# Kernel optimization log

Hardware: AMD Instinct MI355X
Metric: run time of the kernel (lower is better)

The kernel has to match this reference:

```python
import jax, jax.numpy as jnp
import numpy as np

N = 100000
E = 1600000
ROUND = 2


def spmm(src, dst, x):
    # adj.matmul(x) with binary sparse adjacency given as edge list:
    # out[dst] += x[src]
    return jax.ops.segment_sum(x[src], dst, num_segments=N)


def setup_inputs() -> dict:
    key = jax.random.key(0)
    ks = jax.random.split(key, 8)
    x = jax.random.normal(ks[0], (N, 512), dtype=jnp.float32)
    W_embed = jax.random.normal(ks[1], (512, 64), dtype=jnp.float32) * (1.0 / np.sqrt(512))
    b_embed = jnp.zeros((64,), dtype=jnp.float32)
    W_cls = jax.random.normal(ks[2], (448, 40), dtype=jnp.float32) * (1.0 / np.sqrt(448))
    b_cls = jnp.zeros((40,), dtype=jnp.float32)
    adj_src = jax.random.randint(ks[3], (E,), 0, N, dtype=jnp.int32)
    adj_dst = jax.random.randint(ks[4], (E,), 0, N, dtype=jnp.int32)
    adj2_src = jax.random.randint(ks[5], (E,), 0, N, dtype=jnp.int32)
    adj2_dst = jax.random.randint(ks[6], (E,), 0, N, dtype=jnp.int32)
    return {"x": x, "W_embed": W_embed, "b_embed": b_embed, "W_cls": W_cls,
            "b_cls": b_cls, "adj_src": adj_src, "adj_dst": adj_dst,
            "adj2_src": adj2_src, "adj2_dst": adj2_dst}


def reference(x, W_embed, b_embed, W_cls, b_cls, adj_src, adj_dst, adj2_src, adj2_dst):
    # embed: Linear + ReLU
    h = jax.nn.relu(x @ W_embed + b_embed)  # [N, 64]
    hidden_reps = [h]
    for _ in range(ROUND):
        r1 = spmm(adj_src, adj_dst, h)      # 1-hop aggregation
        r2 = spmm(adj2_src, adj2_dst, h)    # 2-hop aggregation
        h = jnp.concatenate([r1, r2], axis=-1)
        hidden_reps.append(h)
    hf = jnp.concatenate(hidden_reps, axis=-1)  # [N, 64*(2^(ROUND+1)-1)] = [N, 448]
    # dropout is identity in eval mode
    logits = hf @ W_cls + b_cls
    return jax.nn.log_softmax(logits, axis=1)
```

## Files before the change

### kernel.cpp

```cpp
#include <hip/hip_runtime.h>
#include <hip/hip_bf16.h>

#define NN 100000
#define EE 1600000
#define NBK 196
#define BSH 9
#define EPB 4096
#define STG 10240

using frag8 = __attribute__((ext_vector_type(8))) short;
using f32x4 = __attribute__((ext_vector_type(4))) float;

__device__ inline unsigned short f2bf(float f) {
    unsigned u = __float_as_uint(f);
    u = u + 0x7FFFu + ((u >> 16) & 1u);
    return (unsigned short)(u >> 16);
}
__device__ inline float bf2f(unsigned short u) {
    return __uint_as_float(((unsigned)u) << 16);
}
__device__ inline unsigned pack_bf16(float a, float b) {
    __hip_bfloat162 h = __float22bfloat162_rn(float2{a, b});
    union { __hip_bfloat162 h2; unsigned u; } c;
    c.h2 = h;
    return c.u;
}


__global__ __launch_bounds__(256) void bhist_k(const int* __restrict__ d1,
                                               const int* __restrict__ d2,
                                               int* __restrict__ bcnt) {
    __shared__ int lh[NBK];
    int adj = blockIdx.y;
    const int* dd = adj ? d2 : d1;
    int t = threadIdx.x;
    for (int i = t; i < NBK; i += 256) lh[i] = 0;
    __syncthreads();
    int e0 = blockIdx.x * EPB;
    #pragma unroll
    for (int k = 0; k < 16; ++k) {
        int e = e0 + k * 256 + t;
        if (e < EE) atomicAdd(&lh[dd[e] >> BSH], 1);
    }
    __syncthreads();
    for (int i = t; i < NBK; i += 256)
        if (lh[i]) atomicAdd(&bcnt[adj * NBK + i], lh[i]);
}

__global__ __launch_bounds__(256) void bscan_k(const int* __restrict__ bcnt,
                                               int* __restrict__ bbase,
                                               int* __restrict__ bcur) {
    int adj = blockIdx.x;
    __shared__ int s[256];
    int t = threadIdx.x;
    int v = (t < NBK) ? bcnt[adj * NBK + t] : 0;
    s[t] = v;
    __syncthreads();
    for (int off = 1; off < 256; off <<= 1) {
        int u = (t >= off) ? s[t - off] : 0;
        __syncthreads();
        s[t] += u;
        __syncthreads();
    }
    if (t < NBK) {
        int ex = s[t] - v;
        bbase[adj * (NBK + 1) + t] = ex;
        bcur[adj * NBK + t] = ex;
    }
    if (t == NBK - 1) bbase[adj * (NBK + 1) + NBK] = s[t];
}

__global__ __launch_bounds__(256) void binA_k(const int* __restrict__ s1,
                                              const int* __restrict__ d1,
                                              const int* __restrict__ s2,
                                              const int* __restrict__ d2,
                                              int* __restrict__ bcur,
                                              uint2* __restrict__ tmp1,
                                              uint2* __restrict__ tmp2) {
    __shared__ int lhist[NBK], lbase[NBK], gbase[NBK], lcur[NBK];
    __shared__ int sscan[256];
    __shared__ int stot;
    __shared__ uint2 stage[EPB];
    int adj = blockIdx.y;
    const int* ss = adj ? s2 : s1;
    const int* dd = adj ? d2 : d1;
    uint2* tmp = adj ? tmp2 : tmp1;
    int t = threadIdx.x;
    for (int i = t; i < NBK; i += 256) { lhist[i] = 0; lcur[i] = 0; }
    __syncthreads();
    int e0 = blockIdx.x * EPB;
    int d[16], s[16];
    #pragma unroll
    for (int k = 0; k < 16; ++k) {
        int e = e0 + k * 256 + t;
        d[k] = (e < EE) ? dd[e] : -1;
        s[k] = (e < EE) ? ss[e] : 0;
        if (d[k] >= 0) atomicAdd(&lhist[d[k] >> BSH], 1);
    }
    __syncthreads();
    int hv = (t < NBK) ? lhist[t] : 0;
    sscan[t] = hv;
    __syncthreads();
    for (int off = 1; off < 256; off <<= 1) {
        int u = (t >= off) ? sscan[t - off] : 0;
        __syncthreads();
        sscan[t] += u;
        __syncthreads();
    }
    if (t < NBK) lbase[t] = sscan[t] - hv;
    if (t == NBK - 1) stot = sscan[t];
    __syncthreads();
    for (int i = t; i < NBK; i += 256)
        gbase[i] = lhist[i] ? atomicAdd(&bcur[adj * NBK + i], lhist[i]) : 0;
    __syncthreads();
    #pragma unroll
    for (int k = 0; k < 16; ++k) {
        if (d[k] >= 0) {
            int b = d[k] >> BSH;
            int pos = lbase[b] + atomicAdd(&lcur[b], 1);
            stage[pos] = make_uint2((unsigned)d[k], (unsigned)s[k]);
        }
    }
    __syncthreads();
    int tot = stot;
    for (int i = t; i < tot; i += 256) {
        uint2 u = stage[i];
        int b = u.x >> BSH;
        tmp[gbase[b] + (i - lbase[b])] = u;
    }
}

__global__ __launch_bounds__(256) void binB_k(const uint2* __restrict__ tmp1,
                                              const uint2* __restrict__ tmp2,
                                              const int* __restrict__ bbase,
                                              int* __restrict__ rs1,
                                              int* __restrict__ rs2,
                                              int* __restrict__ csr1,
                                              int* __restrict__ csr2) {
    __shared__ int cnt[512], cur[512];
    __shared__ int sscan[256];
    __shared__ int stage[STG];
    int adj = blockIdx.y, b = blockIdx.x;
    const uint2* tmp = adj ? tmp2 : tmp1;
    int* rs  = adj ? rs2  : rs1;
    int* csr = adj ? csr2 : csr1;
    int t = threadIdx.x;
    int n0 = b << BSH;
    int n1 = n0 + 512; if (n1 > NN) n1 = NN;
    int nn = n1 - n0;
    int base = bbase[adj * (NBK + 1) + b];
    int count = bbase[adj * (NBK + 1) + b + 1] - base;
    cnt[t] = 0; cnt[t + 256] = 0;
    __syncthreads();
    for (int i = t; i < count; i += 256)
        atomicAdd(&cnt[tmp[base + i].x - n0], 1);
    __syncthreads();
    int c0 = cnt[2 * t], c1 = cnt[2 * t + 1];
    int ps = c0 + c1;
    sscan[t] = ps;
    __syncthreads();
    for (int off = 1; off < 256; off <<= 1) {
        int u = (t >= off) ? sscan[t - off] : 0;
        __syncthreads();
        sscan[t] += u;
        __syncthreads();
    }
    int pe = sscan[t] - ps;
    int e0x = pe, e1x = pe + c0;
    if (2 * t < nn)     rs[n0 + 2 * t]     = base + e0x;
    if (2 * t + 1 < nn) rs[n0 + 2 * t + 1] = base + e1x;
    cur[2 * t] = e0x; cur[2 * t + 1] = e1x;
    if (t == 0 && n1 == NN) rs[NN] = base + count;
    __syncthreads();
    for (int i = t; i < count; i += 256) {
        uint2 u = tmp[base + i];
        int loc = atomicAdd(&cur[u.x - n0], 1);
        if (loc < STG) stage[loc] = (int)u.y;
        else csr[base + loc] = (int)u.y;
    }
    __syncthreads();
    int m = count < STG ? count : STG;
    for (int i = t; i < m; i += 256) csr[base + i] = stage[i];
}


__global__ void wconv_k(const float* __restrict__ W, unsigned short* __restrict__ Wbf) {
    int id = blockIdx.x * 256 + threadIdx.x;
    if (id < 512 * 64) {
        int k = id >> 6, col = id & 63;
        int ch = k >> 3, el = k & 7;
        int cs = (ch & ~15) | ((ch & 15) ^ (col & 7));
        Wbf[col * 512 + cs * 8 + el] = f2bf(W[id]);
    }
}


__global__ void wcls_k(const float* __restrict__ Wc, unsigned short* __restrict__ Wbig) {
    int id = blockIdx.x * 256 + threadIdx.x;
    int k = id >> 7, col = id & 127;
    float v = 0.f;
    if (col < 40) v = Wc[k * 40 + col];
    else if (col < 80)  { if (k >= 64) v = Wc[(192 + k - 64) * 40 + (col - 40)]; }
    else if (col < 120) { if (k >= 64) v = Wc[(320 + k - 64) * 40 + (col - 80)]; }
    int ch = k >> 3, el = k & 7;
    int phys = (ch & ~7) | ((ch & 7) ^ (col & 7));
    Wbig[col * 192 + phys * 8 + el] = f2bf(v);
}


__global__ __launch_bounds__(256) void embed_k(const float* __restrict__ x,
                                               const unsigned short* __restrict__ Wbf,
                                               const float* __restrict__ bias,
                                               unsigned short* __restrict__ hcat) {
    __shared__ unsigned short sA[64 * 128];
    __shared__ unsigned short sW[64 * 128];
    int tid = threadIdx.x;
    int lane = tid & 63, wave = tid >> 6;
    int row0 = blockIdx.x * 64;
    f32x4 acc[4];
    #pragma unroll
    for (int n = 0; n < 4; n++) acc[n] = (f32x4){0.f, 0.f, 0.f, 0.f};

    int ccol = tid & 15;
    int rbase = tid >> 4;

    for (int kt = 0; kt < 4; ++kt) {
        #pragma unroll
        for (int rr = 0; rr < 4; ++rr) {
            int r = rbase + rr * 16;
            int grow = row0 + r;
            float v[8];
            if (grow < NN) {
                const float4* px = (const float4*)(x + (size_t)grow * 512 + kt * 128 + ccol * 8);
                float4 p0 = px[0], p1 = px[1];
                v[0] = p0.x; v[1] = p0.y; v[2] = p0.z; v[3] = p0.w;
                v[4] = p1.x; v[5] = p1.y; v[6] = p1.z; v[7] = p1.w;
            } else {
                #pragma unroll
                for (int i = 0; i < 8; i++) v[i] = 0.f;
            }
            unsigned uu[4];
            #pragma unroll
            for (int i = 0; i < 4; i++)
                uu[i] = pack_bf16(v[2 * i], v[2 * i + 1]);
            int cs = ccol ^ (r & 7);
            uint4 pk; pk.x = uu[0]; pk.y = uu[1]; pk.z = uu[2]; pk.w = uu[3];
            *(uint4*)&sA[(r * 16 + cs) * 8] = pk;
        }
        for (int q = tid; q < 1024; q += 256) {
            int col = q >> 4, c = q & 15;
            ((uint4*)sW)[q] = ((const uint4*)Wbf)[col * 64 + kt * 16 + c];
        }
        __syncthreads();
        #pragma unroll
        for (int kk = 0; kk < 4; ++kk) {
            int ar = wave * 16 + (lane & 15);
            int ac = (kk * 4 + (lane >> 4)) ^ (ar & 7);
            frag8 a = *(const frag8*)&sA[(ar * 16 + ac) * 8];
            #pragma unroll
            for (int n = 0; n < 4; n++) {
                int col = n * 16 + (lane & 15);
                int bc = (kk * 4 + (lane >> 4)) ^ (col & 7);
                frag8 b = *(const frag8*)&sW[(col * 16 + bc) * 8];
                acc[n] = __builtin_amdgcn_mfma_f32_16x16x32_bf16(a, b, acc[n], 0, 0, 0);
            }
        }
        __syncthreads();
    }
    #pragma unroll
    for (int n = 0; n < 4; n++) {
        int col = n * 16 + (lane & 15);
        float bv = bias[col];
        #pragma unroll
        for (int i = 0; i < 4; i++) {
            int r = row0 + wave * 16 + (lane >> 4) * 4 + i;
            if (r < NN) {
                float vv = acc[n][i] + bv;
                vv = vv > 0.f ? vv : 0.f;
                hcat[(size_t)r * 192 + col] = f2bf(vv);
            }
        }
    }
}


__device__ inline void gacc8(float* a, uint4 u) {
    a[0] += bf2f((unsigned short)(u.x & 0xffff));
    a[1] += bf2f((unsigned short)(u.x >> 16));
    a[2] += bf2f((unsigned short)(u.y & 0xffff));
    a[3] += bf2f((unsigned short)(u.y >> 16));
    a[4] += bf2f((unsigned short)(u.z & 0xffff));
    a[5] += bf2f((unsigned short)(u.z >> 16));
    a[6] += bf2f((unsigned short)(u.w & 0xffff));
    a[7] += bf2f((unsigned short)(u.w >> 16));
}


__global__ __launch_bounds__(256) void round1_k(unsigned short* __restrict__ hc,
                                                const int* __restrict__ rs1,
                                                const int* __restrict__ csr1,
                                                const int* __restrict__ rs2,
                                                const int* __restrict__ csr2) {
    int wave = threadIdx.x >> 6, lane = threadIdx.x & 63;
    int row = blockIdx.x * 4 + wave;
    int g = lane >> 3, gl = lane & 7;

    int s1 = rs1[row], e1 = rs1[row + 1];
    int s2 = rs2[row], e2 = rs2[row + 1];
    int c1 = e1 - s1, c2 = e2 - s2;
    int idx1 = 0, idx2 = 0;
    if (lane < c1) idx1 = csr1[s1 + lane];
    if (lane < c2) idx2 = csr2[s2 + lane];
    int cnt1 = c1 < 64 ? c1 : 64, cnt2 = c2 < 64 ? c2 : 64;

    float a1[8] = {0.f, 0.f, 0.f, 0.f, 0.f, 0.f, 0.f, 0.f};
    float a2[8] = {0.f, 0.f, 0.f, 0.f, 0.f, 0.f, 0.f, 0.f};

    {
        int j0 = g, j1 = 8 + g;
        int x10 = __shfl(idx1, j0), x11 = __shfl(idx1, j1);
        int x20 = __shfl(idx2, j0), x21 = __shfl(idx2, j1);
        uint4 u10 = *(const uint4*)(hc + (size_t)x10 * 192 + gl * 8);
        uint4 u11 = *(const uint4*)(hc + (size_t)x11 * 192 + gl * 8);
        uint4 u20 = *(const uint4*)(hc + (size_t)x20 * 192 + gl * 8);
        uint4 u21 = *(const uint4*)(hc + (size_t)x21 * 192 + gl * 8);
        if (j0 < cnt1) gacc8(a1, u10);
        if (j1 < cnt1) gacc8(a1, u11);
        if (j0 < cnt2) gacc8(a2, u20);
        if (j1 < cnt2) gacc8(a2, u21);
    }
    int nq1 = (cnt1 + 7) >> 3, nq2 = (cnt2 + 7) >> 3;
    int nq = nq1 > nq2 ? nq1 : nq2;
    for (int q = 2; q < nq; ++q) {
        int j = q * 8 + g;
        int y1 = __shfl(idx1, j), y2 = __shfl(idx2, j);
        uint4 v1 = *(const uint4*)(hc + (size_t)y1 * 192 + gl * 8);
        uint4 v2 = *(const uint4*)(hc + (size_t)y2 * 192 + gl * 8);
        if (j < cnt1) gacc8(a1, v1);
        if (j < cnt2) gacc8(a2, v2);
    }
    for (int t0 = s1 + 64; t0 < e1; t0 += 64) {
        int rem = e1 - t0;
        int idxv = 0;
        if (lane < rem) idxv = csr1[t0 + lane];
        int cnt = rem < 64 ? rem : 64;
        int nqt = (cnt + 7) >> 3;
        for (int q = 0; q < nqt; ++q) {
            int j = q * 8 + g;
            int s0 = __shfl(idxv, j);
            uint4 u = *(const uint4*)(hc + (size_t)s0 * 192 + gl * 8);
            if (j < cnt) gacc8(a1, u);
        }
    }
    for (int t0 = s2 + 64; t0 < e2; t0 += 64) {
        int rem = e2 - t0;
        int idxv = 0;
        if (lane < rem) idxv = csr2[t0 + lane];
        int cnt = rem < 64 ? rem : 64;
        int nqt = (cnt + 7) >> 3;
        for (int q = 0; q < nqt; ++q) {
            int j = q * 8 + g;
            int s0 = __shfl(idxv, j);
            uint4 u = *(const uint4*)(hc + (size_t)s0 * 192 + gl * 8);
            if (j < cnt) gacc8(a2, u);
        }
    }

    #pragma unroll
    for (int i = 0; i < 8; ++i) {
        a1[i] += __shfl_xor(a1[i], 8);
        a1[i] += __shfl_xor(a1[i], 16);
        a1[i] += __shfl_xor(a1[i], 32);
        a2[i] += __shfl_xor(a2[i], 8);
        a2[i] += __shfl_xor(a2[i], 16);
        a2[i] += __shfl_xor(a2[i], 32);
    }
    if (lane < 8) {
        uint4 o;
        o.x = pack_bf16(a1[0], a1[1]);
        o.y = pack_bf16(a1[2], a1[3]);
        o.z = pack_bf16(a1[4], a1[5]);
        o.w = pack_bf16(a1[6], a1[7]);
        *(uint4*)(hc + (size_t)row * 192 + 64 + lane * 8) = o;
    } else if (lane < 16) {
        int l = lane - 8;
        uint4 o;
        o.x = pack_bf16(a2[0], a2[1]);
        o.y = pack_bf16(a2[2], a2[3]);
        o.z = pack_bf16(a2[4], a2[5]);
        o.w = pack_bf16(a2[6], a2[7]);
        *(uint4*)(hc + (size_t)row * 192 + 128 + l * 8) = o;
    }
}


__global__ __launch_bounds__(256) void gemm_k(const unsigned short* __restrict__ hcat,
                                              const unsigned short* __restrict__ Wbig,
                                              const float* __restrict__ bc,
                                              float* __restrict__ logits,
                                              unsigned short* __restrict__ zcat) {
    __shared__ unsigned short sA[64 * 64];
    __shared__ unsigned short sB[128 * 64];
    int tid = threadIdx.x;
    int lane = tid & 63, wave = tid >> 6;
    int row0 = blockIdx.x * 64;
    f32x4 acc[8];
    #pragma unroll
    for (int n = 0; n < 8; n++) acc[n] = (f32x4){0.f, 0.f, 0.f, 0.f};

    for (int kt = 0; kt < 3; ++kt) {
        #pragma unroll
        for (int q = tid; q < 512; q += 256) {
            int r = q >> 3, c = q & 7;
            int phys = c ^ (r & 7);
            ((uint4*)sA)[r * 8 + phys] = ((const uint4*)hcat)[(size_t)(row0 + r) * 24 + kt * 8 + c];
        }
        #pragma unroll
        for (int q = tid; q < 1024; q += 256) {
            int col = q >> 3, c = q & 7;
            ((uint4*)sB)[q] = ((const uint4*)Wbig)[col * 24 + kt * 8 + c];
        }
        __syncthreads();
        #pragma unroll
        for (int kk = 0; kk < 2; ++kk) {
            int ar = wave * 16 + (lane & 15);
            int ac = (kk * 4 + (lane >> 4)) ^ (ar & 7);
            frag8 a = *(const frag8*)&sA[(ar * 8 + ac) * 8];
            #pragma unroll
            for (int n = 0; n < 8; n++) {
                int col = n * 16 + (lane & 15);
                int bcc = (kk * 4 + (lane >> 4)) ^ (col & 7);
                frag8 b = *(const frag8*)&sB[(col * 8 + bcc) * 8];
                acc[n] = __builtin_amdgcn_mfma_f32_16x16x32_bf16(a, b, acc[n], 0, 0, 0);
            }
        }
        __syncthreads();
    }
    #pragma unroll
    for (int n = 0; n < 8; n++) {
        int col = n * 16 + (lane & 15);
        float bv = (col < 40) ? bc[col] : 0.f;
        #pragma unroll
        for (int i = 0; i < 4; i++) {
            int r = row0 + wave * 16 + (lane >> 4) * 4 + i;
            if (r < NN) {
                float vv = acc[n][i];
                if (col < 40) {
                    logits[(size_t)r * 40 + col] = vv + bv;
                } else if (col < 80) {
                    zcat[(size_t)r * 128 + (col - 40)] = f2bf(vv);
                } else if (col < 120) {
                    zcat[(size_t)r * 128 + 64 + (col - 80)] = f2bf(vv);
                }
            }
        }
    }
}


__global__ __launch_bounds__(256) void round2_k(const unsigned short* __restrict__ zc,
                                                const int* __restrict__ rs1,
                                                const int* __restrict__ csr1,
                                                const int* __restrict__ rs2,
                                                const int* __restrict__ csr2,
                                                float* __restrict__ logits) {
    int wave = threadIdx.x >> 6, lane = threadIdx.x & 63;
    int row = blockIdx.x * 4 + wave;
    int g = lane >> 3, gl = lane & 7;

    int s1 = rs1[row], e1 = rs1[row + 1];
    int s2 = rs2[row], e2 = rs2[row + 1];
    int c1 = e1 - s1, c2 = e2 - s2;
    int idx1 = 0, idx2 = 0;
    if (lane < c1) idx1 = csr1[s1 + lane];
    if (lane < c2) idx2 = csr2[s2 + lane];
    int cnt1 = c1 < 64 ? c1 : 64, cnt2 = c2 < 64 ? c2 : 64;

    size_t zo1 = gl * 8;
    size_t zo2 = 64 + gl * 8;
    float a[8] = {0.f, 0.f, 0.f, 0.f, 0.f, 0.f, 0.f, 0.f};

    {
        int j0 = g, j1 = 8 + g;
        int x10 = __shfl(idx1, j0), x11 = __shfl(idx1, j1);
        int x20 = __shfl(idx2, j0), x21 = __shfl(idx2, j1);
        uint4 u10 = *(const uint4*)(zc + (size_t)x10 * 128 + zo1);
        uint4 u11 = *(const uint4*)(zc + (size_t)x11 * 128 + zo1);
        uint4 u20 = *(const uint4*)(zc + (size_t)x20 * 128 + zo2);
        uint4 u21 = *(const uint4*)(zc + (size_t)x21 * 128 + zo2);
        if (j0 < cnt1) gacc8(a, u10);
        if (j1 < cnt1) gacc8(a, u11);
        if (j0 < cnt2) gacc8(a, u20);
        if (j1 < cnt2) gacc8(a, u21);
    }
    int nq1 = (cnt1 + 7) >> 3, nq2 = (cnt2 + 7) >> 3;
    int nq = nq1 > nq2 ? nq1 : nq2;
    for (int q = 2; q < nq; ++q) {
        int j = q * 8 + g;
        int y1 = __shfl(idx1, j), y2 = __shfl(idx2, j);
        uint4 v1 = *(const uint4*)(zc + (size_t)y1 * 128 + zo1);
        uint4 v2 = *(const uint4*)(zc + (size_t)y2 * 128 + zo2);
        if (j < cnt1) gacc8(a, v1);
        if (j < cnt2) gacc8(a, v2);
    }
    for (int t0 = s1 + 64; t0 < e1; t0 += 64) {
        int rem = e1 - t0;
        int idxv = 0;
        if (lane < rem) idxv = csr1[t0 + lane];
        int cnt = rem < 64 ? rem : 64;
        int nqt = (cnt + 7) >> 3;
        for (int q = 0; q < nqt; ++q) {
            int j = q * 8 + g;
            int s0 = __shfl(idxv, j);
            uint4 u = *(const uint4*)(zc + (size_t)s0 * 128 + zo1);
            if (j < cnt) gacc8(a, u);
        }
    }
    for (int t0 = s2 + 64; t0 < e2; t0 += 64) {
        int rem = e2 - t0;
        int idxv = 0;
        if (lane < rem) idxv = csr2[t0 + lane];
        int cnt = rem < 64 ? rem : 64;
        int nqt = (cnt + 7) >> 3;
        for (int q = 0; q < nqt; ++q) {
            int j = q * 8 + g;
            int s0 = __shfl(idxv, j);
            uint4 u = *(const uint4*)(zc + (size_t)s0 * 128 + zo2);
            if (j < cnt) gacc8(a, u);
        }
    }

    #pragma unroll
    for (int i = 0; i < 8; ++i) {
        a[i] += __shfl_xor(a[i], 8);
        a[i] += __shfl_xor(a[i], 16);
        a[i] += __shfl_xor(a[i], 32);
    }

    bool act = lane < 5;
    float v[8];
    if (act) {
        float4 b0 = *(const float4*)(logits + (size_t)row * 40 + lane * 8);
        float4 b1 = *(const float4*)(logits + (size_t)row * 40 + lane * 8 + 4);
        v[0] = b0.x + a[0]; v[1] = b0.y + a[1]; v[2] = b0.z + a[2]; v[3] = b0.w + a[3];
        v[4] = b1.x + a[4]; v[5] = b1.y + a[5]; v[6] = b1.z + a[6]; v[7] = b1.w + a[7];
    } else {
        #pragma unroll
        for (int i = 0; i < 8; ++i) v[i] = -1e30f;
    }
    float m = fmaxf(fmaxf(fmaxf(v[0], v[1]), fmaxf(v[2], v[3])),
                    fmaxf(fmaxf(v[4], v[5]), fmaxf(v[6], v[7])));
    m = fmaxf(m, __shfl_xor(m, 1));
    m = fmaxf(m, __shfl_xor(m, 2));
    m = fmaxf(m, __shfl_xor(m, 4));
    float es = 0.f;
    if (act) {
        #pragma unroll
        for (int i = 0; i < 8; ++i) es += __expf(v[i] - m);
    }
    es += __shfl_xor(es, 1);
    es += __shfl_xor(es, 2);
    es += __shfl_xor(es, 4);
    float ls = __logf(es);
    if (act) {
        float4 o0, o1;
        o0.x = v[0] - m - ls; o0.y = v[1] - m - ls; o0.z = v[2] - m - ls; o0.w = v[3] - m - ls;
        o1.x = v[4] - m - ls; o1.y = v[5] - m - ls; o1.z = v[6] - m - ls; o1.w = v[7] - m - ls;
        *(float4*)(logits + (size_t)row * 40 + lane * 8)     = o0;
        *(float4*)(logits + (size_t)row * 40 + lane * 8 + 4) = o1;
    }
}


extern "C" void kernel_launch(void* const* d_in, const int* in_sizes, int n_in,
                              void* d_out, int out_size, void* d_ws, size_t ws_size,
                              hipStream_t stream) {
    const float* x       = (const float*)d_in[0];
    const float* W_embed = (const float*)d_in[1];
    const float* b_embed = (const float*)d_in[2];
    const float* W_cls   = (const float*)d_in[3];
    const float* b_cls   = (const float*)d_in[4];
    const int* a1src = (const int*)d_in[5];
    const int* a1dst = (const int*)d_in[6];
    const int* a2src = (const int*)d_in[7];
    const int* a2dst = (const int*)d_in[8];

    float* logits = (float*)d_out;
    float* ws = (float*)d_ws;

    const size_t OFF_HCAT = 0;
    const size_t OFF_ZCAT = 9600000;
    const size_t OFF_RS1  = 16000000;
    const size_t OFF_RS2  = 16100004;
    const size_t OFF_BB   = 16200008;
    const size_t OFF_BC   = 16200402;
    const size_t OFF_BCNT = 16200794;
    const size_t OFF_CSR1 = 16201188;
    const size_t OFF_CSR2 = 17801188;
    const size_t OFF_WBF  = 19401188;
    const size_t OFF_WBIG = 19417572;

    unsigned short* hcat = (unsigned short*)(ws + OFF_HCAT);
    unsigned short* zcat = (unsigned short*)(ws + OFF_ZCAT);
    uint2* tmp1 = (uint2*)(ws + OFF_HCAT);
    uint2* tmp2 = tmp1 + EE;
    int* rs1   = (int*)(ws + OFF_RS1);
    int* rs2   = (int*)(ws + OFF_RS2);
    int* bbase = (int*)(ws + OFF_BB);
    int* bcur  = (int*)(ws + OFF_BC);
    int* bcnt  = (int*)(ws + OFF_BCNT);
    int* csr1  = (int*)(ws + OFF_CSR1);
    int* csr2  = (int*)(ws + OFF_CSR2);
    unsigned short* wbf  = (unsigned short*)(ws + OFF_WBF);
    unsigned short* wbig = (unsigned short*)(ws + OFF_WBIG);

    hipMemsetAsync(ws + OFF_BCNT, 0, 392 * 4, stream);

    const int NBA = (EE + EPB - 1) / EPB;

    bhist_k<<<dim3(NBA, 2), 256, 0, stream>>>(a1dst, a2dst, bcnt);
    bscan_k<<<2, 256, 0, stream>>>(bcnt, bbase, bcur);
    binA_k<<<dim3(NBA, 2), 256, 0, stream>>>(a1src, a1dst, a2src, a2dst, bcur, tmp1, tmp2);
    binB_k<<<dim3(NBK, 2), 256, 0, stream>>>(tmp1, tmp2, bbase, rs1, rs2, csr1, csr2);

    wconv_k<<<128, 256, 0, stream>>>(W_embed, wbf);
    wcls_k<<<96, 256, 0, stream>>>(W_cls, wbig);
    embed_k<<<(NN + 63) / 64, 256, 0, stream>>>(x, wbf, b_embed, hcat);

    round1_k<<<NN / 4, 256, 0, stream>>>(hcat, rs1, csr1, rs2, csr2);
    gemm_k<<<(NN + 63) / 64, 256, 0, stream>>>(hcat, wbig, b_cls, logits, zcat);
    round2_k<<<NN / 4, 256, 0, stream>>>(zcat, rs1, csr1, rs2, csr2, logits);
}
```

Baseline: 298.5 us.

## Pack binned edges into 32-bit words, fuse weight prep, load embed A directly

The binning temp buffer now stores each edge as one 32-bit word: the local destination offset (9 bits) goes in the high bits and the source index (17 bits) in the low bits. This halves the traffic of writing and reading the temp buffer. The two weight-conversion kernels are merged into one launch to save launch overhead. The embed GEMM now loads each lane's x fragment straight from global memory into registers and converts it to bf16 there, dropping the shared-memory A staging and its stores. The trade-off is that global loads are less coalesced per lane (32-byte chunks per row), and the packing relies on source indices fitting in 17 bits.

```diff
diff --git a/kernel.cpp b/kernel.cpp
--- a/kernel.cpp
+++ b/kernel.cpp
@@ -75,8 +75,8 @@
                                               const int* __restrict__ s2,
                                               const int* __restrict__ d2,
                                               int* __restrict__ bcur,
-                                              uint2* __restrict__ tmp1,
-                                              uint2* __restrict__ tmp2) {
+                                              unsigned* __restrict__ tmp1,
+                                              unsigned* __restrict__ tmp2) {
     __shared__ int lhist[NBK], lbase[NBK], gbase[NBK], lcur[NBK];
     __shared__ int sscan[256];
     __shared__ int stot;
@@ -84,7 +84,7 @@
     int adj = blockIdx.y;
     const int* ss = adj ? s2 : s1;
     const int* dd = adj ? d2 : d1;
-    uint2* tmp = adj ? tmp2 : tmp1;
+    unsigned* tmp = adj ? tmp2 : tmp1;
     int t = threadIdx.x;
     for (int i = t; i < NBK; i += 256) { lhist[i] = 0; lcur[i] = 0; }
     __syncthreads();
@@ -126,12 +126,12 @@
     for (int i = t; i < tot; i += 256) {
         uint2 u = stage[i];
         int b = u.x >> BSH;
-        tmp[gbase[b] + (i - lbase[b])] = u;
-    }
-}
-
-__global__ __launch_bounds__(256) void binB_k(const uint2* __restrict__ tmp1,
-                                              const uint2* __restrict__ tmp2,
+        tmp[gbase[b] + (i - lbase[b])] = ((u.x & 511u) << 17) | u.y;
+    }
+}
+
+__global__ __launch_bounds__(256) void binB_k(const unsigned* __restrict__ tmp1,
+                                              const unsigned* __restrict__ tmp2,
                                               const int* __restrict__ bbase,
                                               int* __restrict__ rs1,
                                               int* __restrict__ rs2,
@@ -141,7 +141,7 @@
     __shared__ int sscan[256];
     __shared__ int stage[STG];
     int adj = blockIdx.y, b = blockIdx.x;
-    const uint2* tmp = adj ? tmp2 : tmp1;
+    const unsigned* tmp = adj ? tmp2 : tmp1;
     int* rs  = adj ? rs2  : rs1;
     int* csr = adj ? csr2 : csr1;
     int t = threadIdx.x;
@@ -153,7 +153,7 @@
     cnt[t] = 0; cnt[t + 256] = 0;
     __syncthreads();
     for (int i = t; i < count; i += 256)
-        atomicAdd(&cnt[tmp[base + i].x - n0], 1);
+        atomicAdd(&cnt[tmp[base + i] >> 17], 1);
     __syncthreads();
     int c0 = cnt[2 * t], c1 = cnt[2 * t + 1];
     int ps = c0 + c1;
@@ -173,10 +173,11 @@
     if (t == 0 && n1 == NN) rs[NN] = base + count;
     __syncthreads();
     for (int i = t; i < count; i += 256) {
-        uint2 u = tmp[base + i];
-        int loc = atomicAdd(&cur[u.x - n0], 1);
-        if (loc < STG) stage[loc] = (int)u.y;
-        else csr[base + loc] = (int)u.y;
+        unsigned u = tmp[base + i];
+        int loc = atomicAdd(&cur[u >> 17], 1);
+        int src = (int)(u & 0x1FFFFu);
+        if (loc < STG) stage[loc] = src;
+        else csr[base + loc] = src;
     }
     __syncthreads();
     int m = count < STG ? count : STG;
@@ -184,27 +185,28 @@
 }
 
 
-__global__ void wconv_k(const float* __restrict__ W, unsigned short* __restrict__ Wbf) {
-    int id = blockIdx.x * 256 + threadIdx.x;
-    if (id < 512 * 64) {
-        int k = id >> 6, col = id & 63;
+__global__ void wprep_k(const float* __restrict__ W, unsigned short* __restrict__ Wbf,
+                        const float* __restrict__ Wc, unsigned short* __restrict__ Wbig) {
+    int blk = blockIdx.x;
+    if (blk < 128) {
+        int id = blk * 256 + threadIdx.x;
+        if (id < 512 * 64) {
+            int k = id >> 6, col = id & 63;
+            int ch = k >> 3, el = k & 7;
+            int cs = (ch & ~15) | ((ch & 15) ^ (col & 7));
+            Wbf[col * 512 + cs * 8 + el] = f2bf(W[id]);
+        }
+    } else {
+        int id = (blk - 128) * 256 + threadIdx.x;
+        int k = id >> 7, col = id & 127;
+        float v = 0.f;
+        if (col < 40) v = Wc[k * 40 + col];
+        else if (col < 80)  { if (k >= 64) v = Wc[(192 + k - 64) * 40 + (col - 40)]; }
+        else if (col < 120) { if (k >= 64) v = Wc[(320 + k - 64) * 40 + (col - 80)]; }
         int ch = k >> 3, el = k & 7;
-        int cs = (ch & ~15) | ((ch & 15) ^ (col & 7));
-        Wbf[col * 512 + cs * 8 + el] = f2bf(W[id]);
-    }
-}
-
-
-__global__ void wcls_k(const float* __restrict__ Wc, unsigned short* __restrict__ Wbig) {
-    int id = blockIdx.x * 256 + threadIdx.x;
-    int k = id >> 7, col = id & 127;
-    float v = 0.f;
-    if (col < 40) v = Wc[k * 40 + col];
-    else if (col < 80)  { if (k >= 64) v = Wc[(192 + k - 64) * 40 + (col - 40)]; }
-    else if (col < 120) { if (k >= 64) v = Wc[(320 + k - 64) * 40 + (col - 80)]; }
-    int ch = k >> 3, el = k & 7;
-    int phys = (ch & ~7) | ((ch & 7) ^ (col & 7));
-    Wbig[col * 192 + phys * 8 + el] = f2bf(v);
+        int phys = (ch & ~7) | ((ch & 7) ^ (col & 7));
+        Wbig[col * 192 + phys * 8 + el] = f2bf(v);
+    }
 }
 
 
@@ -212,7 +214,6 @@
                                                const unsigned short* __restrict__ Wbf,
                                                const float* __restrict__ bias,
                                                unsigned short* __restrict__ hcat) {
-    __shared__ unsigned short sA[64 * 128];
     __shared__ unsigned short sW[64 * 128];
     int tid = threadIdx.x;
     int lane = tid & 63, wave = tid >> 6;
@@ -221,32 +222,11 @@
     #pragma unroll
     for (int n = 0; n < 4; n++) acc[n] = (f32x4){0.f, 0.f, 0.f, 0.f};
 
-    int ccol = tid & 15;
-    int rbase = tid >> 4;
+    int arow = row0 + wave * 16 + (lane & 15);
+    bool valid = arow < NN;
+    const float* xrow = x + (size_t)(valid ? arow : 0) * 512 + (lane >> 4) * 8;
 
     for (int kt = 0; kt < 4; ++kt) {
-        #pragma unroll
-        for (int rr = 0; rr < 4; ++rr) {
-            int r = rbase + rr * 16;
-            int grow = row0 + r;
-            float v[8];
-            if (grow < NN) {
-                const float4* px = (const float4*)(x + (size_t)grow * 512 + kt * 128 + ccol * 8);
-                float4 p0 = px[0], p1 = px[1];
-                v[0] = p0.x; v[1] = p0.y; v[2] = p0.z; v[3] = p0.w;
-                v[4] = p1.x; v[5] = p1.y; v[6] = p1.z; v[7] = p1.w;
-            } else {
-                #pragma unroll
-                for (int i = 0; i < 8; i++) v[i] = 0.f;
-            }
-            unsigned uu[4];
-            #pragma unroll
-            for (int i = 0; i < 4; i++)
-                uu[i] = pack_bf16(v[2 * i], v[2 * i + 1]);
-            int cs = ccol ^ (r & 7);
-            uint4 pk; pk.x = uu[0]; pk.y = uu[1]; pk.z = uu[2]; pk.w = uu[3];
-            *(uint4*)&sA[(r * 16 + cs) * 8] = pk;
-        }
         for (int q = tid; q < 1024; q += 256) {
             int col = q >> 4, c = q & 15;
             ((uint4*)sW)[q] = ((const uint4*)Wbf)[col * 64 + kt * 16 + c];
@@ -254,9 +234,18 @@
         __syncthreads();
         #pragma unroll
         for (int kk = 0; kk < 4; ++kk) {
-            int ar = wave * 16 + (lane & 15);
-            int ac = (kk * 4 + (lane >> 4)) ^ (ar & 7);
-            frag8 a = *(const frag8*)&sA[(ar * 16 + ac) * 8];
+            const float4* px = (const float4*)(xrow + kt * 128 + kk * 32);
+            float4 p0 = px[0], p1 = px[1];
+            frag8 a;
+            unsigned* au = (unsigned*)&a;
+            if (valid) {
+                au[0] = pack_bf16(p0.x, p0.y);
+                au[1] = pack_bf16(p0.z, p0.w);
+                au[2] = pack_bf16(p1.x, p1.y);
+                au[3] = pack_bf16(p1.z, p1.w);
+            } else {
+                au[0] = 0; au[1] = 0; au[2] = 0; au[3] = 0;
+            }
             #pragma unroll
             for (int n = 0; n < 4; n++) {
                 int col = n * 16 + (lane & 15);
@@ -602,8 +591,8 @@
 
     unsigned short* hcat = (unsigned short*)(ws + OFF_HCAT);
     unsigned short* zcat = (unsigned short*)(ws + OFF_ZCAT);
-    uint2* tmp1 = (uint2*)(ws + OFF_HCAT);
-    uint2* tmp2 = tmp1 + EE;
+    unsigned* tmp1 = (unsigned*)(ws + OFF_ZCAT);
+    unsigned* tmp2 = tmp1 + EE;
     int* rs1   = (int*)(ws + OFF_RS1);
     int* rs2   = (int*)(ws + OFF_RS2);
     int* bbase = (int*)(ws + OFF_BB);
@@ -623,8 +612,7 @@
     binA_k<<<dim3(NBA, 2), 256, 0, stream>>>(a1src, a1dst, a2src, a2dst, bcur, tmp1, tmp2);
     binB_k<<<dim3(NBK, 2), 256, 0, stream>>>(tmp1, tmp2, bbase, rs1, rs2, csr1, csr2);
 
-    wconv_k<<<128, 256, 0, stream>>>(W_embed, wbf);
-    wcls_k<<<96, 256, 0, stream>>>(W_cls, wbig);
+    wprep_k<<<224, 256, 0, stream>>>(W_embed, wbf, W_cls, wbig);
     embed_k<<<(NN + 63) / 64, 256, 0, stream>>>(x, wbf, b_embed, hcat);
 
     round1_k<<<NN / 4, 256, 0, stream>>>(hcat, rs1, csr1, rs2, csr2);
```

Measured after the change: 284.0 us. 4.9% less time.
